# Performance work log

Hardware: AMD Instinct MI355X
Metric: run time of the kernel (lower is better)

The kernel has to match this reference:

```python
import jax, jax.numpy as jnp
import numpy as np

BLOCK = 64      # InformationEntropyAnalyzer block_size
BINS = 256      # InformationEntropyAnalyzer num_bins
EPS = 1e-12


def setup_inputs() -> dict:
    key = jax.random.key(0)
    x = jax.random.normal(key, (8, 64, 256, 256), dtype=jnp.float32)
    return {"x": x}


def _block_entropy(blocks):
    """Shannon entropy per block, matching np.histogram(density=True) math.

    blocks: (B, n) float32. Returns (B,) float32.
    """
    B, n = blocks.shape
    bmin = jnp.min(blocks, axis=1, keepdims=True)            # (B,1)
    bmax = jnp.max(blocks, axis=1, keepdims=True)            # (B,1)
    width = (bmax - bmin) / BINS                              # uniform bin width
    width_safe = jnp.where(width > 0, width, 1.0)
    # np.histogram: rightmost edge inclusive -> floor + clip reproduces it
    idx = jnp.clip(jnp.floor((blocks - bmin) / width_safe), 0, BINS - 1).astype(jnp.int32)
    row = jnp.arange(B, dtype=jnp.int32)[:, None]
    flat = (row * BINS + idx).reshape(-1)
    counts = jax.ops.segment_sum(
        jnp.ones((B * n,), jnp.float32), flat, num_segments=B * BINS
    ).reshape(B, BINS)
    density = counts / (n * width_safe)                       # density=True normalization
    p = density + EPS
    p = p / jnp.sum(p, axis=1, keepdims=True)
    return -jnp.sum(p * jnp.log2(p), axis=1)


def reference(x):
    """Faithful JAX version of InformationEntropyAnalyzer._compute_4d_entropy.

    Per (n,c) slice: split HxW into BLOCKxBLOCK tiles, compute Shannon entropy
    of the 256-bin histogram of each tile, then bilinearly upsample
    (align_corners=False, i.e. half-pixel, = jax.image.resize 'linear')
    back to (H, W).  Output: (N, C, H, W) entropy map.
    """
    N, C, H, W = x.shape
    nbh, nbw = H // BLOCK, W // BLOCK  # evenly divisible by construction
    blocks = (
        x.reshape(N, C, nbh, BLOCK, nbw, BLOCK)
        .transpose(0, 1, 2, 4, 3, 5)
        .reshape(N * C * nbh * nbw, BLOCK * BLOCK)
    )
    ent = _block_entropy(blocks).reshape(N, C, nbh, nbw)
    # F.interpolate(mode='bilinear', align_corners=False) == half-pixel linear resize
    return jax.image.resize(ent, (N, C, H, W), method='linear')
```

## Files before the change

kernel.cpp:

```cpp
#include <hip/hip_runtime.h>

#define NBINS 256
#define EPSF 1e-12f

typedef float v4f __attribute__((ext_vector_type(4)));

__global__ __launch_bounds__(256, 2) void fused_kernel(const float* __restrict__ x,
                                                       float* __restrict__ out) {
    const int nc   = blockIdx.x;
    const int t    = threadIdx.x;
    const int lane = t & 63;
    const int wave = t >> 6;

    __shared__ unsigned int hist[4][NBINS];
    __shared__ float ent_s[16];

    const float* rbase = x + ((size_t)nc << 16) + (size_t)wave * (64 * 256);

    for (int col = 0; col < 4; ++col) {
        const float* tbase = rbase + col * 64;

        v4f v[16];
        float lmin = INFINITY, lmax = -INFINITY;
#pragma unroll
        for (int k = 0; k < 16; ++k) {
            const int f   = lane + (k << 6);
            const int row = f >> 4;
            const int c4  = f & 15;
            v[k] = *reinterpret_cast<const v4f*>(tbase + (size_t)row * 256 + c4 * 4);
            lmin = fminf(lmin, fminf(fminf(v[k].x, v[k].y), fminf(v[k].z, v[k].w)));
            lmax = fmaxf(lmax, fmaxf(fmaxf(v[k].x, v[k].y), fmaxf(v[k].z, v[k].w)));
        }
#pragma unroll
        for (int off = 32; off > 0; off >>= 1) {
            lmin = fminf(lmin, __shfl_xor(lmin, off));
            lmax = fmaxf(lmax, __shfl_xor(lmax, off));
        }

        uint4 z; z.x = z.y = z.z = z.w = 0u;
        reinterpret_cast<uint4*>(hist[wave])[lane] = z;

        const float width = (lmax - lmin) * (1.0f / NBINS);
        const float wsafe = (width > 0.0f) ? width : 1.0f;
        const float inv   = 1.0f / wsafe;

        unsigned int* h = hist[wave];
#pragma unroll
        for (int k = 0; k < 16; ++k) {
            float vals[4] = {v[k].x, v[k].y, v[k].z, v[k].w};
#pragma unroll
            for (int j = 0; j < 4; ++j) {
                float f   = floorf((vals[j] - lmin) * inv);
                int   bin = (int)fminf(fmaxf(f, 0.0f), 255.0f);
                atomicAdd(&h[bin], 1u);
            }
        }

        const uint4 c   = reinterpret_cast<const uint4*>(hist[wave])[lane];
        const float den = 4096.0f * wsafe;
        const float p0 = (float)c.x / den + EPSF;
        const float p1 = (float)c.y / den + EPSF;
        const float p2 = (float)c.z / den + EPSF;
        const float p3 = (float)c.w / den + EPSF;
        float s = p0 + p1 + p2 + p3;
#pragma unroll
        for (int off = 32; off > 0; off >>= 1) s += __shfl_xor(s, off);
        const float itot = 1.0f / s;
        const float q0 = p0 * itot, q1 = p1 * itot, q2 = p2 * itot, q3 = p3 * itot;
        float e = q0 * log2f(q0) + q1 * log2f(q1) + q2 * log2f(q2) + q3 * log2f(q3);
#pragma unroll
        for (int off = 32; off > 0; off >>= 1) e += __shfl_xor(e, off);
        if (lane == 0) ent_s[(wave << 2) + col] = -e;
    }
    __syncthreads();

    const int x4 = t & 63;
    const int yy = wave;

    const int ix = (int)floorf(((x4 << 2) + 0.5f) * 0.015625f - 0.5f);
    const int x0 = max(ix, 0), x1 = min(ix + 1, 3);
    v4f wv[4];
#pragma unroll
    for (int j = 0; j < 4; ++j) {
        const float fx = ((x4 << 2) + j + 0.5f) * 0.015625f - 0.5f;
        const float wx = fx - floorf(fx);
        const float a  = 1.0f - wx, bb = wx;
        wv[j].x = ((x0 == 0) ? a : 0.0f) + ((x1 == 0) ? bb : 0.0f);
        wv[j].y = ((x0 == 1) ? a : 0.0f) + ((x1 == 1) ? bb : 0.0f);
        wv[j].z = ((x0 == 2) ? a : 0.0f) + ((x1 == 2) ? bb : 0.0f);
        wv[j].w = ((x0 == 3) ? a : 0.0f) + ((x1 == 3) ? bb : 0.0f);
    }

    const v4f* er = reinterpret_cast<const v4f*>(ent_s);
    v4f* out4 = reinterpret_cast<v4f*>(out) + ((size_t)nc << 14);
#pragma unroll 8
    for (int it = 0; it < 64; ++it) {
        const int   y   = (it << 2) + yy;
        const float fy  = (y + 0.5f) * 0.015625f - 0.5f;
        const float fiy = floorf(fy);
        const float wy  = fy - fiy;
        const int   iy  = (int)fiy;
        const int   y0  = max(iy, 0), y1 = min(iy + 1, 3);
        const float wy0 = 1.0f - wy;

        const v4f r0 = er[y0];
        const v4f r1 = er[y1];
        v4f rv = r0 * wy0 + r1 * wy;
        v4f o;
        o.x = rv.x * wv[0].x + rv.y * wv[0].y + rv.z * wv[0].z + rv.w * wv[0].w;
        o.y = rv.x * wv[1].x + rv.y * wv[1].y + rv.z * wv[1].z + rv.w * wv[1].w;
        o.z = rv.x * wv[2].x + rv.y * wv[2].y + rv.z * wv[2].z + rv.w * wv[2].w;
        o.w = rv.x * wv[3].x + rv.y * wv[3].y + rv.z * wv[3].z + rv.w * wv[3].w;
        __builtin_nontemporal_store(o, out4 + (y << 6) + x4);
    }
}

extern "C" void kernel_launch(void* const* d_in, const int* in_sizes, int n_in,
                              void* d_out, int out_size, void* d_ws, size_t ws_size,
                              hipStream_t stream) {
    const float* x   = (const float*)d_in[0];
    float*       out = (float*)d_out;
    fused_kernel<<<512, 256, 0, stream>>>(x, out);
}
```

Baseline: 49.66 us.

## Double-buffer tile loads across columns and simplify bin index arithmetic

Unrolls the four per-wave tile iterations and uses two register buffers, so the global loads for the next tile are issued before the current tile is processed. This hides memory latency behind histogram work. It also replaces floor/clamp with a single fma plus a truncating cast and min, and turns the density division into a multiply. Register pressure rises from 16 to 32 vectors per thread under launch bounds (256,2), which risks spills. The truncation gives a different bin than floor when the value is slightly negative due to rounding, but the cast still maps that to bin 0.

```diff
diff --git a/kernel.cpp b/kernel.cpp
--- a/kernel.cpp
+++ b/kernel.cpp
@@ -16,62 +16,80 @@
     __shared__ float ent_s[16];
 
     const float* rbase = x + ((size_t)nc << 16) + (size_t)wave * (64 * 256);
+    unsigned int* h = hist[wave];
 
-    for (int col = 0; col < 4; ++col) {
-        const float* tbase = rbase + col * 64;
+    v4f va[16], vb[16];
 
-        v4f v[16];
-        float lmin = INFINITY, lmax = -INFINITY;
-#pragma unroll
-        for (int k = 0; k < 16; ++k) {
-            const int f   = lane + (k << 6);
-            const int row = f >> 4;
-            const int c4  = f & 15;
-            v[k] = *reinterpret_cast<const v4f*>(tbase + (size_t)row * 256 + c4 * 4);
-            lmin = fminf(lmin, fminf(fminf(v[k].x, v[k].y), fminf(v[k].z, v[k].w)));
-            lmax = fmaxf(lmax, fmaxf(fmaxf(v[k].x, v[k].y), fmaxf(v[k].z, v[k].w)));
-        }
-#pragma unroll
-        for (int off = 32; off > 0; off >>= 1) {
-            lmin = fminf(lmin, __shfl_xor(lmin, off));
-            lmax = fmaxf(lmax, __shfl_xor(lmax, off));
-        }
+#define ISSUE(buf, col)                                                           \
+    _Pragma("unroll")                                                             \
+    for (int k = 0; k < 16; ++k) {                                                \
+        const int f = lane + (k << 6);                    \
+        buf[k] = *reinterpret_cast<const v4f*>(                                   \
+            rbase + (col) * 64 + (size_t)(f >> 4) * 256 + (f & 15) * 4);          \
+    }
 
-        uint4 z; z.x = z.y = z.z = z.w = 0u;
-        reinterpret_cast<uint4*>(hist[wave])[lane] = z;
+#define PROCESS(buf, col)                                                         \
+    {                                                                             \
+        float lmin = INFINITY, lmax = -INFINITY;                                  \
+        _Pragma("unroll")                                                         \
+        for (int k = 0; k < 16; ++k) {                                            \
+            lmin = fminf(lmin, fminf(fminf(buf[k].x, buf[k].y),                   \
+                                     fminf(buf[k].z, buf[k].w)));                 \
+            lmax = fmaxf(lmax, fmaxf(fmaxf(buf[k].x, buf[k].y),                   \
+                                     fmaxf(buf[k].z, buf[k].w)));                 \
+        }                                                                         \
+        _Pragma("unroll")                                                         \
+        for (int off = 32; off > 0; off >>= 1) {                                  \
+            lmin = fminf(lmin, __shfl_xor(lmin, off));                            \
+            lmax = fmaxf(lmax, __shfl_xor(lmax, off));                            \
+        }                                                                         \
+        uint4 z; z.x = z.y = z.z = z.w = 0u;       \
+        reinterpret_cast<uint4*>(h)[lane] = z;                                    \
+        const float width = (lmax - lmin) * (1.0f / NBINS);                       \
+        const float wsafe = (width > 0.0f) ? width : 1.0f;                        \
+        const float inv   = 1.0f / wsafe;                                         \
+        const float coff  = -lmin * inv;                                          \
+        _Pragma("unroll")                                                         \
+        for (int k = 0; k < 16; ++k) {                                            \
+            float vals[4] = {buf[k].x, buf[k].y, buf[k].z, buf[k].w};             \
+            _Pragma("unroll")                                                     \
+            for (int j = 0; j < 4; ++j) {                                         \
+                      \
+                int bin = (int)fmaf(vals[j], inv, coff);                          \
+                bin = min(bin, 255);                                              \
+                atomicAdd(&h[bin], 1u);                                           \
+            }                                                                     \
+        }                                                                         \
+        const uint4 c    = reinterpret_cast<const uint4*>(h)[lane];               \
+        const float pden = inv * (1.0f / 4096.0f);            \
+        const float p0 = (float)c.x * pden + EPSF;                                \
+        const float p1 = (float)c.y * pden + EPSF;                                \
+        const float p2 = (float)c.z * pden + EPSF;                                \
+        const float p3 = (float)c.w * pden + EPSF;                                \
+        float s = p0 + p1 + p2 + p3;                                              \
+        _Pragma("unroll")                                                         \
+        for (int off = 32; off > 0; off >>= 1) s += __shfl_xor(s, off);           \
+        const float itot = 1.0f / s;                                              \
+        const float q0 = p0 * itot, q1 = p1 * itot;                               \
+        const float q2 = p2 * itot, q3 = p3 * itot;                               \
+        float e = q0 * log2f(q0) + q1 * log2f(q1)                                 \
+                + q2 * log2f(q2) + q3 * log2f(q3);                                \
+        _Pragma("unroll")                                                         \
+        for (int off = 32; off > 0; off >>= 1) e += __shfl_xor(e, off);           \
+        if (lane == 0) ent_s[(wave << 2) + (col)] = -e;                           \
+    }
 
-        const float width = (lmax - lmin) * (1.0f / NBINS);
-        const float wsafe = (width > 0.0f) ? width : 1.0f;
-        const float inv   = 1.0f / wsafe;
+    ISSUE(va, 0)
+    ISSUE(vb, 1)
+    PROCESS(va, 0)
+    ISSUE(va, 2)
+    PROCESS(vb, 1)
+    ISSUE(vb, 3)
+    PROCESS(va, 2)
+    PROCESS(vb, 3)
+#undef ISSUE
+#undef PROCESS
 
-        unsigned int* h = hist[wave];
-#pragma unroll
-        for (int k = 0; k < 16; ++k) {
-            float vals[4] = {v[k].x, v[k].y, v[k].z, v[k].w};
-#pragma unroll
-            for (int j = 0; j < 4; ++j) {
-                float f   = floorf((vals[j] - lmin) * inv);
-                int   bin = (int)fminf(fmaxf(f, 0.0f), 255.0f);
-                atomicAdd(&h[bin], 1u);
-            }
-        }
-
-        const uint4 c   = reinterpret_cast<const uint4*>(hist[wave])[lane];
-        const float den = 4096.0f * wsafe;
-        const float p0 = (float)c.x / den + EPSF;
-        const float p1 = (float)c.y / den + EPSF;
-        const float p2 = (float)c.z / den + EPSF;
-        const float p3 = (float)c.w / den + EPSF;
-        float s = p0 + p1 + p2 + p3;
-#pragma unroll
-        for (int off = 32; off > 0; off >>= 1) s += __shfl_xor(s, off);
-        const float itot = 1.0f / s;
-        const float q0 = p0 * itot, q1 = p1 * itot, q2 = p2 * itot, q3 = p3 * itot;
-        float e = q0 * log2f(q0) + q1 * log2f(q1) + q2 * log2f(q2) + q3 * log2f(q3);
-#pragma unroll
-        for (int off = 32; off > 0; off >>= 1) e += __shfl_xor(e, off);
-        if (lane == 0) ent_s[(wave << 2) + col] = -e;
-    }
     __syncthreads();
 
     const int x4 = t & 63;
```

Measured after the change: 48.00 us. 1.03x faster.
